# Performance work log

Measured on AMD Instinct MI355X. Metric: run time of the kernel, lower is better.

## Reference

```python
import jax, jax.numpy as jnp
import numpy as np

NUM_NODES = 10000
NUM_FEAT = 32
HIDDEN = 64
OUT_FEAT = 16
NUM_EDGES = 160000
SEQ_LEN = 12
BATCH = 1


def _gcn_conv(x, W, b, row, col, n):
    # PyG GCNConv: h = D^-1/2 (A+I) D^-1/2 (x @ W) + b
    # x: (n, T, F_in), row/col: (E+n,) with self-loops already appended
    h = x @ W                                              # (n, T, H)
    deg = jax.ops.segment_sum(jnp.ones_like(col, dtype=h.dtype), col, num_segments=n)
    dis = 1.0 / jnp.sqrt(jnp.maximum(deg, 1.0))            # deg >= 1 due to self-loops
    norm = dis[row] * dis[col]                             # (E+n,)
    msg = h[row] * norm[:, None, None]                     # gather + scale
    return jax.ops.segment_sum(msg, col, num_segments=n) + b


def _lstm_layer(x, wih, whh, bih, bhh):
    # x: (N, T, F); PyTorch gate order i, f, g, o
    H = whh.shape[1]
    Nn = x.shape[0]
    bias = bih + bhh

    def step(carry, xt):
        h, c = carry
        g = xt @ wih.T + h @ whh.T + bias
        i, f, gg, o = jnp.split(g, 4, axis=-1)
        c = jax.nn.sigmoid(f) * c + jax.nn.sigmoid(i) * jnp.tanh(gg)
        h = jax.nn.sigmoid(o) * jnp.tanh(c)
        return (h, c), h

    h0 = jnp.zeros((Nn, H), x.dtype)
    c0 = jnp.zeros((Nn, H), x.dtype)
    _, ys = jax.lax.scan(step, (h0, c0), jnp.transpose(x, (1, 0, 2)))
    return jnp.transpose(ys, (1, 0, 2))                    # (N, T, H)


def setup_inputs() -> dict:
    key = jax.random.key(0)
    ks = jax.random.split(key, 16)
    s_in = 1.0 / np.sqrt(NUM_FEAT)
    s_h = 1.0 / np.sqrt(HIDDEN)
    inp = {
        "x": jax.random.normal(ks[0], (BATCH, SEQ_LEN, NUM_NODES, NUM_FEAT), jnp.float32),
        "edge_index": jax.random.randint(ks[1], (2, NUM_EDGES), 0, NUM_NODES, dtype=jnp.int64),
        "gw0": jax.random.normal(ks[2], (NUM_FEAT, HIDDEN), jnp.float32) * s_in,
        "gb0": jnp.zeros((HIDDEN,), jnp.float32),
        "gw1": jax.random.normal(ks[3], (HIDDEN, HIDDEN), jnp.float32) * s_h,
        "gb1": jnp.zeros((HIDDEN,), jnp.float32),
        "wih0": jax.random.normal(ks[4], (4 * HIDDEN, HIDDEN), jnp.float32) * s_h,
        "whh0": jax.random.normal(ks[5], (4 * HIDDEN, HIDDEN), jnp.float32) * s_h,
        "bih0": jax.random.normal(ks[6], (4 * HIDDEN,), jnp.float32) * s_h,
        "bhh0": jax.random.normal(ks[7], (4 * HIDDEN,), jnp.float32) * s_h,
        "wih1": jax.random.normal(ks[8], (4 * HIDDEN, HIDDEN), jnp.float32) * s_h,
        "whh1": jax.random.normal(ks[9], (4 * HIDDEN, HIDDEN), jnp.float32) * s_h,
        "bih1": jax.random.normal(ks[10], (4 * HIDDEN,), jnp.float32) * s_h,
        "bhh1": jax.random.normal(ks[11], (4 * HIDDEN,), jnp.float32) * s_h,
        "fc_w": jax.random.normal(ks[12], (OUT_FEAT, HIDDEN), jnp.float32) * s_h,
        "fc_b": jnp.zeros((OUT_FEAT,), jnp.float32),
    }
    return inp


def reference(x, edge_index, gw0, gb0, gw1, gb1, wih0, whh0, bih0, bhh0,
              wih1, whh1, bih1, bhh1, fc_w, fc_b):
    B, T, n, F = x.shape
    BN = B * n
    # (B, T, N, F) -> (B, N, T, F) -> (B*N, T, F); the per-timestep GCN loop in
    # the original is batched over T here (same math, edge_index is time-invariant).
    xs = jnp.transpose(x, (0, 2, 1, 3)).reshape(BN, T, F)
    loops = jnp.arange(BN, dtype=edge_index.dtype)
    row = jnp.concatenate([edge_index[0], loops])
    col = jnp.concatenate([edge_index[1], loops])
    h = jax.nn.relu(_gcn_conv(xs, gw0, gb0, row, col, BN))
    h = jax.nn.relu(_gcn_conv(h, gw1, gb1, row, col, BN))
    h = _lstm_layer(h, wih0, whh0, bih0, bhh0)
    h = _lstm_layer(h, wih1, whh1, bih1, bhh1)
    out = h[:, -1, :] @ fc_w.T + fc_b                      # last timestep only
    return out.reshape(B, n, OUT_FEAT)
```

## Files before the change

kernel.cpp:

```cpp
#include <hip/hip_runtime.h>
#include <hip/hip_bf16.h>

constexpr int kNN  = 10000;
constexpr int kTT  = 12;
constexpr int kFIN = 32;
constexpr int kHH  = 64;
constexpr int kH4  = 256;
constexpr int kOUT = 16;
constexpr int kNE  = 160000;

typedef _Float16 half8 __attribute__((ext_vector_type(8)));
typedef _Float16 half4 __attribute__((ext_vector_type(4)));
typedef _Float16 half2t __attribute__((ext_vector_type(2)));
typedef float floatx4 __attribute__((ext_vector_type(4)));

__device__ __forceinline__ float sigf(float x){ return 1.f/(1.f+__expf(-x)); }
__device__ __forceinline__ float tanh_fast(float x){
  float xc = fminf(fmaxf(x,-30.f),30.f);
  float e = __expf(-2.f*xc);
  return (1.f-e)/(1.f+e);
}

__global__ void k_detect_cast(const int* __restrict__ ei, int* __restrict__ anyf,
                              const float* __restrict__ x, _Float16* __restrict__ xh){
  int a = 0;
  for (int i = blockIdx.x*256 + threadIdx.x; i < kNE; i += gridDim.x*256)
    a |= ei[2*i+1];
  unsigned long long m = __ballot(a != 0);
  if ((threadIdx.x & 63) == 0 && m) atomicOr(anyf, 1);
  const int NV = kNN*kTT*kFIN/4;
  for (int i = blockIdx.x*256 + threadIdx.x; i < NV; i += gridDim.x*256){
    float4 v = *(const float4*)&x[4*i];
    half4 h;
    h[0]=(_Float16)v.x; h[1]=(_Float16)v.y; h[2]=(_Float16)v.z; h[3]=(_Float16)v.w;
    *(half4*)&xh[4*i] = h;
  }
}

__global__ void k_deg(const int* __restrict__ ei, const int* __restrict__ anyf,
                      int* __restrict__ cnt){
  int e = blockIdx.x*256 + threadIdx.x;
  if (e >= kNE) return;
  int c = (anyf[0]==0) ? ei[2*(kNE+e)] : ei[kNE+e];
  atomicAdd(&cnt[c], 1);
}

__global__ void k_scan(const int* __restrict__ cnt, int* __restrict__ offs,
                       float* __restrict__ dis){
  __shared__ int wsum[4];
  int tid = threadIdx.x;
  const int CH = (kNN + 255)/256;
  int lo = tid*CH, hi = min(lo+CH, kNN);
  int s = 0;
  for (int i = lo; i < hi; ++i) s += cnt[i];
  int orig = s;
  int lane = tid & 63, wv = tid >> 6;
  #pragma unroll
  for (int d = 1; d < 64; d <<= 1){
    int v = __shfl_up(s, d, 64);
    if (lane >= d) s += v;
  }
  if (lane == 63) wsum[wv] = s;
  __syncthreads();
  int add = 0;
  for (int k2 = 0; k2 < wv; ++k2) add += wsum[k2];
  int run = s - orig + add;
  for (int i = lo; i < hi; ++i){ offs[i] = run; run += cnt[i]; }
  if (hi == kNN) offs[kNN] = run;
  for (int i = tid; i < kNN; i += 256) dis[i] = rsqrtf((float)(cnt[i]+1));
}

__global__ void k_scatter(const int* __restrict__ ei, const int* __restrict__ anyf,
                          const int* __restrict__ offs, int* __restrict__ cur,
                          const float* __restrict__ dis,
                          int2* __restrict__ edat){
  int e = blockIdx.x*256 + threadIdx.x;
  if (e >= kNE) return;
  int f = (anyf[0]==0);
  int r = f ? ei[2*e]         : ei[e];
  int c = f ? ei[2*(kNE+e)]   : ei[kNE+e];
  int p = offs[c] + atomicAdd(&cur[c], 1);
  edat[p] = make_int2(r, __float_as_int(dis[r]*dis[c]));
}

template<int F>
__global__ __launch_bounds__(256) void k_agg(const _Float16* __restrict__ hin,
                     _Float16* __restrict__ hout,
                     const float* __restrict__ dis,
                     const int* __restrict__ offs, const int2* __restrict__ edat){
  constexpr int LPF = F/2;
  constexpr int TPW = 64/LPF;
  int wid = threadIdx.x >> 6, lane = threadIdx.x & 63;
  int gw = blockIdx.x*4 + wid;
  int tq = gw / kNN, n = gw - tq*kNN;
  int fp = lane & (LPF-1), tsub = lane / LPF;
  int t = TPW*tq + tsub;
  const _Float16* hb = hin + (size_t)t*kNN*F;
  float d = dis[n], ws = d*d;
  half2t sv = *(const half2t*)&hb[(size_t)n*F + 2*fp];
  float a0 = ws*(float)sv[0], a1 = ws*(float)sv[1];
  int e0 = __builtin_amdgcn_readfirstlane(offs[n]);
  int e1 = __builtin_amdgcn_readfirstlane(offs[n+1]);
  int e = e0;
  for (; e + 8 <= e1; e += 8){
    int2 d8[8];
    #pragma unroll
    for (int u = 0; u < 8; ++u) d8[u] = edat[e+u];
    half2t v[8];
    #pragma unroll
    for (int u = 0; u < 8; ++u) v[u] = *(const half2t*)&hb[(size_t)d8[u].x*F + 2*fp];
    #pragma unroll
    for (int u = 0; u < 8; ++u){
      float wu = __int_as_float(d8[u].y);
      a0 = fmaf(wu, (float)v[u][0], a0);
      a1 = fmaf(wu, (float)v[u][1], a1);
    }
  }
  for (; e < e1; ++e){
    int2 du = edat[e];
    float wu = __int_as_float(du.y);
    half2t vu = *(const half2t*)&hb[(size_t)du.x*F + 2*fp];
    a0 = fmaf(wu, (float)vu[0], a0);
    a1 = fmaf(wu, (float)vu[1], a1);
  }
  half2t o; o[0] = (_Float16)a0; o[1] = (_Float16)a1;
  *(half2t*)&hout[((size_t)t*kNN + n)*F + 2*fp] = o;
}

template<int K, int N, bool NM>
__global__ __launch_bounds__(256) void k_gemm(const _Float16* __restrict__ in,
                      const float* __restrict__ Wg, const float* __restrict__ bias,
                      _Float16* __restrict__ out){
  constexpr int COLG = N/4;
  constexpr int ROWG = 256/COLG;
  constexpr int MR   = 4;
  constexpr int MTILE= ROWG*MR;
  constexpr int AP   = K + 4;
  __shared__ float Wl[K*N];
  __shared__ float Al[MTILE*AP];
  int tid = threadIdx.x;
  int m0 = blockIdx.x*MTILE;
  for (int idx = tid; idx < MTILE*K/8; idx += 256){
    int r = idx/(K/8), k8 = idx - r*(K/8);
    half8 v = *(const half8*)&in[(size_t)(m0 + r)*K + k8*8];
    float* dst = &Al[r*AP + k8*8];
    #pragma unroll
    for (int j = 0; j < 8; ++j) dst[j] = (float)v[j];
  }
  for (int idx = tid; idx < K*N; idx += 256) Wl[idx] = Wg[idx];
  __syncthreads();
  int cg = tid % COLG, rg = tid / COLG;
  int c0 = cg*4, r0 = rg*MR;
  float acc[MR][4];
  #pragma unroll
  for (int r=0;r<MR;++r){acc[r][0]=0.f;acc[r][1]=0.f;acc[r][2]=0.f;acc[r][3]=0.f;}
  #pragma unroll 2
  for (int k = 0; k < K; k += 4){
    float4 wv[4];
    #pragma unroll
    for (int kk = 0; kk < 4; ++kk) wv[kk] = *(const float4*)&Wl[(k+kk)*N + c0];
    #pragma unroll
    for (int r = 0; r < MR; ++r){
      float4 a4 = *(const float4*)&Al[(r0+r)*AP + k];
      acc[r][0] = fmaf(a4.x, wv[0].x, acc[r][0]);
      acc[r][1] = fmaf(a4.x, wv[0].y, acc[r][1]);
      acc[r][2] = fmaf(a4.x, wv[0].z, acc[r][2]);
      acc[r][3] = fmaf(a4.x, wv[0].w, acc[r][3]);
      acc[r][0] = fmaf(a4.y, wv[1].x, acc[r][0]);
      acc[r][1] = fmaf(a4.y, wv[1].y, acc[r][1]);
      acc[r][2] = fmaf(a4.y, wv[1].z, acc[r][2]);
      acc[r][3] = fmaf(a4.y, wv[1].w, acc[r][3]);
      acc[r][0] = fmaf(a4.z, wv[2].x, acc[r][0]);
      acc[r][1] = fmaf(a4.z, wv[2].y, acc[r][1]);
      acc[r][2] = fmaf(a4.z, wv[2].z, acc[r][2]);
      acc[r][3] = fmaf(a4.z, wv[2].w, acc[r][3]);
      acc[r][0] = fmaf(a4.w, wv[3].x, acc[r][0]);
      acc[r][1] = fmaf(a4.w, wv[3].y, acc[r][1]);
      acc[r][2] = fmaf(a4.w, wv[3].z, acc[r][2]);
      acc[r][3] = fmaf(a4.w, wv[3].w, acc[r][3]);
    }
  }
  float4 bb = *(const float4*)&bias[c0];
  #pragma unroll
  for (int r = 0; r < MR; ++r){
    half4 hv;
    hv[0]=(_Float16)fmaxf(acc[r][0]+bb.x, 0.f);
    hv[1]=(_Float16)fmaxf(acc[r][1]+bb.y, 0.f);
    hv[2]=(_Float16)fmaxf(acc[r][2]+bb.z, 0.f);
    hv[3]=(_Float16)fmaxf(acc[r][3]+bb.w, 0.f);
    int m = m0 + r0 + r;
    size_t oi;
    if (NM){ int t = m/kNN, n = m - t*kNN; oi = ((size_t)n*kTT + t)*N + c0; }
    else    oi = (size_t)m*N + c0;
    *(half4*)&out[oi] = hv;
  }
}

__global__ __launch_bounds__(512) void k_rec2(const _Float16* __restrict__ xin,
                     const float* __restrict__ wih0, const float* __restrict__ whh0,
                     const float* __restrict__ bih0, const float* __restrict__ bhh0,
                     const float* __restrict__ wih1, const float* __restrict__ whh1,
                     const float* __restrict__ bih1, const float* __restrict__ bhh1,
                     const float* __restrict__ fcw, const float* __restrict__ fcb,
                     float* __restrict__ out){
  constexpr int LP = 72;
  __shared__ _Float16 h0b[2][2][16*LP];
  __shared__ _Float16 h1b[2][2][16*LP];
  int tid = threadIdx.x, w = tid >> 6, lane = tid & 63;
  int lo = lane & 15, hi4 = lane >> 4;
  int layer = w >> 2, wl = w & 3;
  int nb0 = blockIdx.x*32;

  const float* wih = layer ? wih1 : wih0;
  const float* whh = layer ? whh1 : whh0;
  const float* bi_ = layer ? bih1 : bih0;
  const float* bh_ = layer ? bhh1 : bhh0;

  half8 BI[4][2], BH[4][2];
  #pragma unroll
  for (int q = 0; q < 4; ++q){
    int row = q*kHH + wl*16 + lo;
    #pragma unroll
    for (int kt = 0; kt < 2; ++kt){
      const float* pi = wih + (size_t)row*kHH + kt*32 + hi4*8;
      const float* ph = whh + (size_t)row*kHH + kt*32 + hi4*8;
      half8 fi, fh;
      #pragma unroll
      for (int j = 0; j < 8; ++j){ fi[j] = (_Float16)pi[j]; fh[j] = (_Float16)ph[j]; }
      BI[q][kt] = fi; BH[q][kt] = fh;
    }
  }
  float bias[4];
  #pragma unroll
  for (int q = 0; q < 4; ++q){
    int col = q*kHH + wl*16 + lo;
    bias[q] = bi_[col] + bh_[col];
  }
  half8 FW[2];
  if (w == 4 || w == 5){
    #pragma unroll
    for (int kt = 0; kt < 2; ++kt){
      const float* pf = fcw + (size_t)lo*kHH + kt*32 + hi4*8;
      half8 f;
      #pragma unroll
      for (int j = 0; j < 8; ++j) f[j] = (_Float16)pf[j];
      FW[kt] = f;
    }
  }

  float c[2][4];
  #pragma unroll
  for (int u = 0; u < 2; ++u){c[u][0]=0.f;c[u][1]=0.f;c[u][2]=0.f;c[u][3]=0.f;}
  half8 ax[2][2], ah[2][2], axn[2][2];

  const _Float16* xrow[2];
  #pragma unroll
  for (int u = 0; u < 2; ++u)
    xrow[u] = xin + (size_t)min(nb0 + u*16 + lo, kNN-1)*kTT*kHH;
  if (layer == 0){
    #pragma unroll
    for (int u = 0; u < 2; ++u)
      #pragma unroll
      for (int kt = 0; kt < 2; ++kt)
        axn[u][kt] = *(const half8*)&xrow[u][kt*32 + hi4*8];
  }

  for (int i = 0; i < 13; ++i){
    int t = layer ? i-1 : i;
    bool act = layer ? (i >= 1) : (i < 12);
    if (act){
      #pragma unroll
      for (int u = 0; u < 2; ++u){
        if (layer == 0){
          ax[u][0] = axn[u][0]; ax[u][1] = axn[u][1];
          if (t < kTT-1){
            #pragma unroll
            for (int kt = 0; kt < 2; ++kt)
              axn[u][kt] = *(const half8*)&xrow[u][(size_t)(t+1)*kHH + kt*32 + hi4*8];
          }
        }
        floatx4 acc[4];
        #pragma unroll
        for (int q = 0; q < 4; ++q){
          floatx4 a = {0.f,0.f,0.f,0.f};
          a = __builtin_amdgcn_mfma_f32_16x16x32_f16(ax[u][0], BI[q][0], a, 0,0,0);
          a = __builtin_amdgcn_mfma_f32_16x16x32_f16(ax[u][1], BI[q][1], a, 0,0,0);
          acc[q] = a;
        }
        if (t > 0){
          #pragma unroll
          for (int q = 0; q < 4; ++q){
            floatx4 a = acc[q];
            a = __builtin_amdgcn_mfma_f32_16x16x32_f16(ah[u][0], BH[q][0], a, 0,0,0);
            a = __builtin_amdgcn_mfma_f32_16x16x32_f16(ah[u][1], BH[q][1], a, 0,0,0);
            acc[q] = a;
          }
        }
        _Float16* hb = layer ? &h1b[u][t & 1][0] : &h0b[u][t & 1][0];
        #pragma unroll
        for (int r = 0; r < 4; ++r){
          float gi = acc[0][r] + bias[0];
          float gf = acc[1][r] + bias[1];
          float gg = acc[2][r] + bias[2];
          float go = acc[3][r] + bias[3];
          float ii = sigf(gi), ff = sigf(gf), gt = tanh_fast(gg), oo = sigf(go);
          c[u][r] = ff*c[u][r] + ii*gt;
          float hn = oo * tanh_fast(c[u][r]);
          hb[(hi4*4 + r)*LP + wl*16 + lo] = (_Float16)hn;
        }
      }
    }
    __syncthreads();
    if (layer == 0){
      if (i < 11){
        #pragma unroll
        for (int u = 0; u < 2; ++u){
          const _Float16* rb = &h0b[u][i & 1][0];
          #pragma unroll
          for (int kt = 0; kt < 2; ++kt)
            ah[u][kt] = *(const half8*)&rb[lo*LP + kt*32 + hi4*8];
        }
      }
    } else {
      if (i < 12){
        #pragma unroll
        for (int u = 0; u < 2; ++u){
          const _Float16* rb = &h0b[u][i & 1][0];
          #pragma unroll
          for (int kt = 0; kt < 2; ++kt)
            ax[u][kt] = *(const half8*)&rb[lo*LP + kt*32 + hi4*8];
        }
      }
      if (i >= 1 && i < 12){
        #pragma unroll
        for (int u = 0; u < 2; ++u){
          const _Float16* rb = &h1b[u][(i-1) & 1][0];
          #pragma unroll
          for (int kt = 0; kt < 2; ++kt)
            ah[u][kt] = *(const half8*)&rb[lo*LP + kt*32 + hi4*8];
        }
      }
    }
  }
  if (w == 4 || w == 5){
    int u = w - 4;
    const _Float16* rb = &h1b[u][1][0];
    half8 a0 = *(const half8*)&rb[lo*LP + 0*32 + hi4*8];
    half8 a1 = *(const half8*)&rb[lo*LP + 1*32 + hi4*8];
    floatx4 a = {0.f,0.f,0.f,0.f};
    a = __builtin_amdgcn_mfma_f32_16x16x32_f16(a0, FW[0], a, 0,0,0);
    a = __builtin_amdgcn_mfma_f32_16x16x32_f16(a1, FW[1], a, 0,0,0);
    float bo = fcb[lo];
    #pragma unroll
    for (int r = 0; r < 4; ++r){
      int n = nb0 + u*16 + hi4*4 + r;
      if (n < kNN) out[(size_t)n*kOUT + lo] = a[r] + bo;
    }
  }
}

extern "C" void kernel_launch(void* const* d_in, const int* in_sizes, int n_in,
                              void* d_out, int out_size, void* d_ws, size_t ws_size,
                              hipStream_t stream){
  const float* x    = (const float*)d_in[0];
  const int*   ei   = (const int*)  d_in[1];
  const float* gw0  = (const float*)d_in[2];
  const float* gb0  = (const float*)d_in[3];
  const float* gw1  = (const float*)d_in[4];
  const float* gb1  = (const float*)d_in[5];
  const float* wih0 = (const float*)d_in[6];
  const float* whh0 = (const float*)d_in[7];
  const float* bih0 = (const float*)d_in[8];
  const float* bhh0 = (const float*)d_in[9];
  const float* wih1 = (const float*)d_in[10];
  const float* whh1 = (const float*)d_in[11];
  const float* bih1 = (const float*)d_in[12];
  const float* bhh1 = (const float*)d_in[13];
  const float* fcw  = (const float*)d_in[14];
  const float* fcb  = (const float*)d_in[15];
  float* out = (float*)d_out;

  char* ws = (char*)d_ws;
  size_t p = 0;
  auto carve = [&](size_t bytes)->char*{
    char* r = ws + p;
    p += (bytes + 255) & ~(size_t)255;
    return r;
  };
  int*   anyf = (int*)  carve(256);
  int*   cnt  = (int*)  carve(sizeof(int)*kNN);
  int*   cur  = (int*)  carve(sizeof(int)*kNN);
  size_t zbytes = p;
  int*   offs = (int*)  carve(sizeof(int)*(kNN+1));
  float* dis  = (float*)carve(sizeof(float)*kNN);
  int2*  edat = (int2*) carve(sizeof(int2)*kNE);
  _Float16* xh   = (_Float16*)carve(sizeof(_Float16)*(size_t)kNN*kTT*kFIN);
  _Float16* aggX = (_Float16*)carve(sizeof(_Float16)*(size_t)kNN*kTT*kFIN);
  _Float16* bufA = (_Float16*)carve(sizeof(_Float16)*(size_t)kNN*kTT*kHH);
  _Float16* bufB = (_Float16*)carve(sizeof(_Float16)*(size_t)kNN*kTT*kHH);
  (void)ws_size; (void)in_sizes; (void)n_in; (void)out_size;

  hipMemsetAsync(ws, 0, zbytes, stream);
  k_detect_cast<<<120, 256, 0, stream>>>(ei, anyf, x, xh);
  k_deg    <<<(kNE+255)/256, 256, 0, stream>>>(ei, anyf, cnt);
  k_scan   <<<1, 256, 0, stream>>>(cnt, offs, dis);
  k_scatter<<<(kNE+255)/256, 256, 0, stream>>>(ei, anyf, offs, cur, dis, edat);

  k_agg<kFIN><<<(kNN*(kTT/4))/4, 256, 0, stream>>>(xh, aggX, dis, offs, edat);
  k_gemm<kFIN, kHH, false><<<(kNN*kTT)/64, 256, 0, stream>>>(aggX, gw0, gb0, bufB);
  k_agg<kHH><<<(kNN*(kTT/2))/4, 256, 0, stream>>>(bufB, bufA, dis, offs, edat);
  k_gemm<kHH, kHH, true><<<(kNN*kTT)/64, 256, 0, stream>>>(bufA, gw1, gb1, bufB);

  k_rec2<<<(kNN+31)/32, 512, 0, stream>>>(bufB, wih0, whh0, bih0, bhh0,
                                          wih1, whh1, bih1, bhh1, fcw, fcb, out);
}
```

Before: 328.3 us.

## Run both LSTM layers in the same warps with smaller 16-node blocks

The two-layer LSTM kernel moves from 512-thread blocks, where separate warps ran each layer in a software pipeline over 32 nodes, to 256-thread blocks over 16 nodes. Each warp now holds the weights for both layers and computes layer 0 then layer 1 at each timestep. The whole input sequence for the block is staged into LDS up front instead of prefetched per step. This gives twice as many blocks with fewer threads each, which may help occupancy and latency hiding. In exchange it adds a second barrier per timestep, serialises the two layers inside each warp, and raises register pressure from holding both layers' weights.

```diff
diff --git a/kernel.cpp b/kernel.cpp
--- a/kernel.cpp
+++ b/kernel.cpp
@@ -196,48 +196,51 @@
   }
 }
 
-__global__ __launch_bounds__(512) void k_rec2(const _Float16* __restrict__ xin,
+__global__ __launch_bounds__(256) void k_rec3(const _Float16* __restrict__ xin,
                      const float* __restrict__ wih0, const float* __restrict__ whh0,
                      const float* __restrict__ bih0, const float* __restrict__ bhh0,
                      const float* __restrict__ wih1, const float* __restrict__ whh1,
                      const float* __restrict__ bih1, const float* __restrict__ bhh1,
                      const float* __restrict__ fcw, const float* __restrict__ fcb,
                      float* __restrict__ out){
-  constexpr int LP = 72;
-  __shared__ _Float16 h0b[2][2][16*LP];
-  __shared__ _Float16 h1b[2][2][16*LP];
+  constexpr int XP  = kTT*kHH + 8;
+  constexpr int LPH = 72;
+  __shared__ _Float16 xl[16*XP];
+  __shared__ _Float16 h0l[16*LPH];
+  __shared__ _Float16 h1l[16*LPH];
   int tid = threadIdx.x, w = tid >> 6, lane = tid & 63;
   int lo = lane & 15, hi4 = lane >> 4;
-  int layer = w >> 2, wl = w & 3;
-  int nb0 = blockIdx.x*32;
-
-  const float* wih = layer ? wih1 : wih0;
-  const float* whh = layer ? whh1 : whh0;
-  const float* bi_ = layer ? bih1 : bih0;
-  const float* bh_ = layer ? bhh1 : bhh0;
-
-  half8 BI[4][2], BH[4][2];
+  int nb = blockIdx.x*16;
+
+  for (int idx = tid; idx < 16*(kTT*kHH/8); idx += 256){
+    int r = idx/(kTT*kHH/8), c8 = idx - r*(kTT*kHH/8);
+    *(half8*)&xl[r*XP + c8*8] = *(const half8*)&xin[((size_t)(nb+r)*kTT*kHH) + c8*8];
+  }
+
+  half8 BI0[4][2], BH0[4][2], BI1[4][2], BH1[4][2];
+  float bias0[4], bias1[4];
   #pragma unroll
-  for (int q = 0; q < 4; ++q){
-    int row = q*kHH + wl*16 + lo;
+  for (int g4 = 0; g4 < 4; ++g4){
+    int row = g4*kHH + w*16 + lo;
+    bias0[g4] = bih0[row] + bhh0[row];
+    bias1[g4] = bih1[row] + bhh1[row];
     #pragma unroll
     for (int kt = 0; kt < 2; ++kt){
-      const float* pi = wih + (size_t)row*kHH + kt*32 + hi4*8;
-      const float* ph = whh + (size_t)row*kHH + kt*32 + hi4*8;
-      half8 fi, fh;
+      const float* p0 = wih0 + (size_t)row*kHH + kt*32 + hi4*8;
+      const float* q0 = whh0 + (size_t)row*kHH + kt*32 + hi4*8;
+      const float* p1 = wih1 + (size_t)row*kHH + kt*32 + hi4*8;
+      const float* q1 = whh1 + (size_t)row*kHH + kt*32 + hi4*8;
+      half8 a, b, c2, d2;
       #pragma unroll
-      for (int j = 0; j < 8; ++j){ fi[j] = (_Float16)pi[j]; fh[j] = (_Float16)ph[j]; }
-      BI[q][kt] = fi; BH[q][kt] = fh;
-    }
-  }
-  float bias[4];
-  #pragma unroll
-  for (int q = 0; q < 4; ++q){
-    int col = q*kHH + wl*16 + lo;
-    bias[q] = bi_[col] + bh_[col];
+      for (int j = 0; j < 8; ++j){
+        a[j]=(_Float16)p0[j]; b[j]=(_Float16)q0[j];
+        c2[j]=(_Float16)p1[j]; d2[j]=(_Float16)q1[j];
+      }
+      BI0[g4][kt]=a; BH0[g4][kt]=b; BI1[g4][kt]=c2; BH1[g4][kt]=d2;
+    }
   }
   half8 FW[2];
-  if (w == 4 || w == 5){
+  if (w == 0){
     #pragma unroll
     for (int kt = 0; kt < 2; ++kt){
       const float* pf = fcw + (size_t)lo*kHH + kt*32 + hi4*8;
@@ -248,114 +251,87 @@
     }
   }
 
-  float c[2][4];
-  #pragma unroll
-  for (int u = 0; u < 2; ++u){c[u][0]=0.f;c[u][1]=0.f;c[u][2]=0.f;c[u][3]=0.f;}
-  half8 ax[2][2], ah[2][2], axn[2][2];
-
-  const _Float16* xrow[2];
-  #pragma unroll
-  for (int u = 0; u < 2; ++u)
-    xrow[u] = xin + (size_t)min(nb0 + u*16 + lo, kNN-1)*kTT*kHH;
-  if (layer == 0){
-    #pragma unroll
-    for (int u = 0; u < 2; ++u)
+  float c0s[4] = {0.f,0.f,0.f,0.f}, c1s[4] = {0.f,0.f,0.f,0.f};
+  half8 ah0[2], ah1[2];
+  __syncthreads();
+
+  for (int t = 0; t < kTT; ++t){
+    half8 ax0 = *(const half8*)&xl[lo*XP + t*kHH + hi4*8];
+    half8 ax1 = *(const half8*)&xl[lo*XP + t*kHH + 32 + hi4*8];
+    floatx4 acc[4];
+    #pragma unroll
+    for (int g4 = 0; g4 < 4; ++g4){
+      floatx4 a = {0.f,0.f,0.f,0.f};
+      a = __builtin_amdgcn_mfma_f32_16x16x32_f16(ax0, BI0[g4][0], a, 0,0,0);
+      a = __builtin_amdgcn_mfma_f32_16x16x32_f16(ax1, BI0[g4][1], a, 0,0,0);
+      acc[g4] = a;
+    }
+    if (t > 0){
       #pragma unroll
-      for (int kt = 0; kt < 2; ++kt)
-        axn[u][kt] = *(const half8*)&xrow[u][kt*32 + hi4*8];
-  }
-
-  for (int i = 0; i < 13; ++i){
-    int t = layer ? i-1 : i;
-    bool act = layer ? (i >= 1) : (i < 12);
-    if (act){
+      for (int g4 = 0; g4 < 4; ++g4){
+        floatx4 a = acc[g4];
+        a = __builtin_amdgcn_mfma_f32_16x16x32_f16(ah0[0], BH0[g4][0], a, 0,0,0);
+        a = __builtin_amdgcn_mfma_f32_16x16x32_f16(ah0[1], BH0[g4][1], a, 0,0,0);
+        acc[g4] = a;
+      }
+    }
+    #pragma unroll
+    for (int r = 0; r < 4; ++r){
+      float gi = acc[0][r] + bias0[0];
+      float gf = acc[1][r] + bias0[1];
+      float gg = acc[2][r] + bias0[2];
+      float go = acc[3][r] + bias0[3];
+      float ii = sigf(gi), ff = sigf(gf), gt = tanh_fast(gg), oo = sigf(go);
+      c0s[r] = ff*c0s[r] + ii*gt;
+      float hn = oo * tanh_fast(c0s[r]);
+      h0l[(hi4*4 + r)*LPH + w*16 + lo] = (_Float16)hn;
+    }
+    __syncthreads();
+    #pragma unroll
+    for (int kt = 0; kt < 2; ++kt)
+      ah0[kt] = *(const half8*)&h0l[lo*LPH + kt*32 + hi4*8];
+
+    #pragma unroll
+    for (int g4 = 0; g4 < 4; ++g4){
+      floatx4 a = {0.f,0.f,0.f,0.f};
+      a = __builtin_amdgcn_mfma_f32_16x16x32_f16(ah0[0], BI1[g4][0], a, 0,0,0);
+      a = __builtin_amdgcn_mfma_f32_16x16x32_f16(ah0[1], BI1[g4][1], a, 0,0,0);
+      acc[g4] = a;
+    }
+    if (t > 0){
       #pragma unroll
-      for (int u = 0; u < 2; ++u){
-        if (layer == 0){
-          ax[u][0] = axn[u][0]; ax[u][1] = axn[u][1];
-          if (t < kTT-1){
-            #pragma unroll
-            for (int kt = 0; kt < 2; ++kt)
-              axn[u][kt] = *(const half8*)&xrow[u][(size_t)(t+1)*kHH + kt*32 + hi4*8];
-          }
-        }
-        floatx4 acc[4];
-        #pragma unroll
-        for (int q = 0; q < 4; ++q){
-          floatx4 a = {0.f,0.f,0.f,0.f};
-          a = __builtin_amdgcn_mfma_f32_16x16x32_f16(ax[u][0], BI[q][0], a, 0,0,0);
-          a = __builtin_amdgcn_mfma_f32_16x16x32_f16(ax[u][1], BI[q][1], a, 0,0,0);
-          acc[q] = a;
-        }
-        if (t > 0){
-          #pragma unroll
-          for (int q = 0; q < 4; ++q){
-            floatx4 a = acc[q];
-            a = __builtin_amdgcn_mfma_f32_16x16x32_f16(ah[u][0], BH[q][0], a, 0,0,0);
-            a = __builtin_amdgcn_mfma_f32_16x16x32_f16(ah[u][1], BH[q][1], a, 0,0,0);
-            acc[q] = a;
-          }
-        }
-        _Float16* hb = layer ? &h1b[u][t & 1][0] : &h0b[u][t & 1][0];
-        #pragma unroll
-        for (int r = 0; r < 4; ++r){
-          float gi = acc[0][r] + bias[0];
-          float gf = acc[1][r] + bias[1];
-          float gg = acc[2][r] + bias[2];
-          float go = acc[3][r] + bias[3];
-          float ii = sigf(gi), ff = sigf(gf), gt = tanh_fast(gg), oo = sigf(go);
-          c[u][r] = ff*c[u][r] + ii*gt;
-          float hn = oo * tanh_fast(c[u][r]);
-          hb[(hi4*4 + r)*LP + wl*16 + lo] = (_Float16)hn;
-        }
+      for (int g4 = 0; g4 < 4; ++g4){
+        floatx4 a = acc[g4];
+        a = __builtin_amdgcn_mfma_f32_16x16x32_f16(ah1[0], BH1[g4][0], a, 0,0,0);
+        a = __builtin_amdgcn_mfma_f32_16x16x32_f16(ah1[1], BH1[g4][1], a, 0,0,0);
+        acc[g4] = a;
       }
     }
+    #pragma unroll
+    for (int r = 0; r < 4; ++r){
+      float gi = acc[0][r] + bias1[0];
+      float gf = acc[1][r] + bias1[1];
+      float gg = acc[2][r] + bias1[2];
+      float go = acc[3][r] + bias1[3];
+      float ii = sigf(gi), ff = sigf(gf), gt = tanh_fast(gg), oo = sigf(go);
+      c1s[r] = ff*c1s[r] + ii*gt;
+      float hn = oo * tanh_fast(c1s[r]);
+      h1l[(hi4*4 + r)*LPH + w*16 + lo] = (_Float16)hn;
+    }
     __syncthreads();
-    if (layer == 0){
-      if (i < 11){
-        #pragma unroll
-        for (int u = 0; u < 2; ++u){
-          const _Float16* rb = &h0b[u][i & 1][0];
-          #pragma unroll
-          for (int kt = 0; kt < 2; ++kt)
-            ah[u][kt] = *(const half8*)&rb[lo*LP + kt*32 + hi4*8];
-        }
-      }
-    } else {
-      if (i < 12){
-        #pragma unroll
-        for (int u = 0; u < 2; ++u){
-          const _Float16* rb = &h0b[u][i & 1][0];
-          #pragma unroll
-          for (int kt = 0; kt < 2; ++kt)
-            ax[u][kt] = *(const half8*)&rb[lo*LP + kt*32 + hi4*8];
-        }
-      }
-      if (i >= 1 && i < 12){
-        #pragma unroll
-        for (int u = 0; u < 2; ++u){
-          const _Float16* rb = &h1b[u][(i-1) & 1][0];
-          #pragma unroll
-          for (int kt = 0; kt < 2; ++kt)
-            ah[u][kt] = *(const half8*)&rb[lo*LP + kt*32 + hi4*8];
-        }
-      }
-    }
-  }
-  if (w == 4 || w == 5){
-    int u = w - 4;
-    const _Float16* rb = &h1b[u][1][0];
-    half8 a0 = *(const half8*)&rb[lo*LP + 0*32 + hi4*8];
-    half8 a1 = *(const half8*)&rb[lo*LP + 1*32 + hi4*8];
+    #pragma unroll
+    for (int kt = 0; kt < 2; ++kt)
+      ah1[kt] = *(const half8*)&h1l[lo*LPH + kt*32 + hi4*8];
+  }
+
+  if (w == 0){
     floatx4 a = {0.f,0.f,0.f,0.f};
-    a = __builtin_amdgcn_mfma_f32_16x16x32_f16(a0, FW[0], a, 0,0,0);
-    a = __builtin_amdgcn_mfma_f32_16x16x32_f16(a1, FW[1], a, 0,0,0);
+    a = __builtin_amdgcn_mfma_f32_16x16x32_f16(ah1[0], FW[0], a, 0,0,0);
+    a = __builtin_amdgcn_mfma_f32_16x16x32_f16(ah1[1], FW[1], a, 0,0,0);
     float bo = fcb[lo];
     #pragma unroll
-    for (int r = 0; r < 4; ++r){
-      int n = nb0 + u*16 + hi4*4 + r;
-      if (n < kNN) out[(size_t)n*kOUT + lo] = a[r] + bo;
-    }
+    for (int r = 0; r < 4; ++r)
+      out[(size_t)(nb + hi4*4 + r)*kOUT + lo] = a[r] + bo;
   }
 }
 
@@ -411,6 +387,6 @@
   k_agg<kHH><<<(kNN*(kTT/2))/4, 256, 0, stream>>>(bufB, bufA, dis, offs, edat);
   k_gemm<kHH, kHH, true><<<(kNN*kTT)/64, 256, 0, stream>>>(bufA, gw1, gb1, bufB);
 
-  k_rec2<<<(kNN+31)/32, 512, 0, stream>>>(bufB, wih0, whh0, bih0, bhh0,
-                                          wih1, whh1, bih1, bhh1, fcw, fcb, out);
-}
+  k_rec3<<<kNN/16, 256, 0, stream>>>(bufB, wih0, whh0, bih0, bhh0,
+                                     wih1, whh1, bih1, bhh1, fcw, fcb, out);
+}
```

Result: no change. 330.6 us (+0.7%).
